# Kernel tuning notes

Measured on AMD Instinct MI355X. Metric: run time of the kernel, lower is better.

Reference implementation:

```python
import jax, jax.numpy as jnp
import numpy as np

N_NODES = 100000
N_EDGES = 1600000  # undirected edges (each pair listed once, no self loops)
IN_CH, HID, OUT_CH = 512, 64, 32
MU, P, K = 0.1, 1.5, 2
EPS = 1e-8


def setup_inputs() -> dict:
    key = jax.random.key(0)
    k_x, k_src, k_off, k_w1, k_w2 = jax.random.split(key, 5)
    x = jax.random.normal(k_x, (N_NODES, IN_CH), dtype=jnp.float32)
    # undirected edge list with no self loops: dst = (src + offset) % N, offset in [1, N)
    src = jax.random.randint(k_src, (N_EDGES,), 0, N_NODES)
    off = jax.random.randint(k_off, (N_EDGES,), 1, N_NODES)
    dst = (src + off) % N_NODES
    edge_index = jnp.stack([src, dst], axis=0)
    # parameters (lin1 of pGNNNet, lin1 of pGNNConv)
    W1 = jax.random.normal(k_w1, (IN_CH, HID), dtype=jnp.float32) / np.sqrt(IN_CH)
    b1 = jnp.zeros((HID,), dtype=jnp.float32)
    W2 = jax.random.normal(k_w2, (HID, OUT_CH), dtype=jnp.float32) / np.sqrt(HID)
    b2 = jnp.zeros((OUT_CH,), dtype=jnp.float32)
    return {"x": x, "edge_index": edge_index, "W1": W1, "b1": b1, "W2": W2, "b2": b2}


def reference(x, edge_index, W1, b1, W2, b2):
    src, dst = edge_index[0], edge_index[1]
    n = x.shape[0]
    # pGNNNet.lin1 + ReLU (dropout is identity in eval mode)
    h = jax.nn.relu(x @ W1 + b1)                   # [N, HID]
    # pGNNConv.lin1 applied before propagation
    f = h @ W2 + b2                                # [N, OUT]
    # degrees of the symmetric adjacency (no self loops)
    ones = jnp.ones(src.shape, dtype=f.dtype)
    deg = jax.ops.segment_sum(ones, src, num_segments=n) + \
          jax.ops.segment_sum(ones, dst, num_segments=n)
    dinv = jnp.where(deg > 0, 1.0 / deg, 0.0)      # [N]
    dis = jnp.sqrt(dinv)                           # D^{-1/2}
    out = f
    for _ in range(K):
        gs = out * dis[:, None]                    # D^{-1/2} f
        g = gs[src] - gs[dst]                      # graph gradient per edge [E, OUT]
        # edge reweighting: ||grad||^{p-2}
        w = jnp.power(jnp.sum(g * g, axis=1) + EPS, (P - 2.0) * 0.5)   # [E]
        # row sums of M (symmetric, M_ij = w_e)
        s = jax.ops.segment_sum(w, src, num_segments=n) + \
            jax.ops.segment_sum(w, dst, num_segments=n)
        alpha = 1.0 / (s * dinv + MU)              # [N]
        beta = MU * alpha
        # (D^{-1/2} M D^{-1/2} out): scatter-add messages both directions
        m = w[:, None]
        agg = jax.ops.segment_sum(m * gs[dst], src, num_segments=n) + \
              jax.ops.segment_sum(m * gs[src], dst, num_segments=n)
        out = alpha[:, None] * (dis[:, None] * agg) + beta[:, None] * f
    return jax.nn.log_softmax(out, axis=1)
```

## Files before the change

### kernel.cpp

```cpp
#include <hip/hip_runtime.h>
#include <hip/hip_bf16.h>
#include <math.h>

#define N_NODES 100000
#define N_EDGES 1600000
#define IN_CH 512
#define HID 64
#define OUT_CH 32
#define MU 0.1f
#define EPS 1e-8f

#define HE (2 * N_EDGES)
#define ABLK 625
#define EPT 20
#define NBUCK 391
#define BCAP 9216
#define PCAP 10240

typedef short bf16x8 __attribute__((ext_vector_type(8)));
typedef unsigned short us8 __attribute__((ext_vector_type(8)));
typedef float f32x4 __attribute__((ext_vector_type(4)));

__device__ __forceinline__ short f2bf(float f) {
  __hip_bfloat16 h = __float2bfloat16(f);
  return *reinterpret_cast<short*>(&h);
}
__device__ __forceinline__ float bf2f(unsigned short u) {
  unsigned int b = ((unsigned int)u) << 16;
  return __uint_as_float(b);
}

__global__ __launch_bounds__(256) void k_scatter(
    const int* __restrict__ ends, const float* __restrict__ W1,
    const float* __restrict__ W2, short* __restrict__ w1t,
    short* __restrict__ w2t, int* __restrict__ gcur, int* __restrict__ pairs) {
  const int t = threadIdx.x;
  const int b = blockIdx.x;
  {
    const int i = b * 256 + t;
    if (i < IN_CH * HID) {
      int k = i / HID, c = i % HID;
      w1t[c * IN_CH + k] = f2bf(W1[i]);
    } else if (i < IN_CH * HID + HID * OUT_CH) {
      int j = i - IN_CH * HID;
      w2t[(j % OUT_CH) * HID + (j / OUT_CH)] = f2bf(W2[j]);
    }
  }
  __shared__ int cnt[NBUCK];
  for (int i = t; i < NBUCK; i += 256) cnt[i] = 0;
  __syncthreads();
  const int base = b * (256 * EPT);
  int us[EPT];
  #pragma unroll
  for (int j = 0; j < EPT; ++j) us[j] = ends[base + j * 256 + t];
  #pragma unroll
  for (int j = 0; j < EPT; ++j) atomicAdd(&cnt[us[j] >> 8], 1);
  __syncthreads();
  for (int i = t; i < NBUCK; i += 256) {
    const int c = cnt[i];
    cnt[i] = c > 0 ? i * BCAP + atomicAdd(&gcur[i], c) : 0;
  }
  __syncthreads();
  #pragma unroll
  for (int j = 0; j < EPT; ++j) {
    const int i = base + j * 256 + t;
    const int u = us[j];
    const int nb = ends[i < N_EDGES ? i + N_EDGES : i - N_EDGES];
    pairs[atomicAdd(&cnt[u >> 8], 1)] = ((u & 255) << 24) | nb;
  }
}

__global__ __launch_bounds__(256) void k_csr(const int* __restrict__ pairs,
                                             const int* __restrict__ gcur,
                                             int2* __restrict__ degrs,
                                             int* __restrict__ adj) {
  __shared__ int pl[PCAP];
  __shared__ int cnt[256];
  __shared__ int sh[256];
  const int b = blockIdx.x, t = threadIdx.x;
  const int pbase = b * BCAP;
  const int psz = gcur[b];
  const bool fits = psz <= PCAP;
  cnt[t] = 0;
  __syncthreads();
  if (fits) {
    for (int i = t; i < psz; i += 256) {
      int p = pairs[pbase + i];
      pl[i] = p;
      atomicAdd(&cnt[((unsigned)p) >> 24], 1);
    }
  } else {
    for (int i = t; i < psz; i += 256)
      atomicAdd(&cnt[((unsigned)pairs[pbase + i]) >> 24], 1);
  }
  __syncthreads();
  const int d = cnt[t];
  sh[t] = d;
  __syncthreads();
  for (int s = 1; s < 256; s <<= 1) {
    int a = t >= s ? sh[t - s] : 0;
    __syncthreads();
    sh[t] += a;
    __syncthreads();
  }
  const int rs = pbase + sh[t] - d;
  const int v = (b << 8) + t;
  if (v < N_NODES) degrs[v] = make_int2(d, rs);
  __syncthreads();
  cnt[t] = rs;
  __syncthreads();
  for (int i = t; i < psz; i += 256) {
    const int p = fits ? pl[i] : pairs[pbase + i];
    adj[atomicAdd(&cnt[((unsigned)p) >> 24], 1)] = p & 0xFFFFFF;
  }
}

__global__ __launch_bounds__(256) void k_mlp(
    const float* __restrict__ x, const short* __restrict__ w1t,
    const float* __restrict__ b1, const short* __restrict__ w2t,
    const float* __restrict__ b2, const int2* __restrict__ degrs,
    float* __restrict__ f, unsigned short* __restrict__ gs) {
  __shared__ short ht[4][16][72];
  __shared__ __align__(16) float xstage[4][2080];

  const int t = threadIdx.x;
  const int w = t >> 6;
  const int l = t & 63;
  const int lr = l & 15;
  const int kq = l >> 4;
  const int band = blockIdx.x * 64 + w * 16;

  float* xb = xstage[w];
  const int srow = l >> 5;
  const int sgran = l & 31;

  f32x4 acc1[4] = {};
  const char* fb = (const char*)xb + (lr >> 1) * 1040 + (lr & 1) * 512 + kq * 32;

  for (int c = 0; c < 4; ++c) {
    asm volatile("" ::: "memory");
    #pragma unroll
    for (int i = 0; i < 8; ++i) {
      int grow = band + 2 * i + srow;
      grow = grow < N_NODES ? grow : N_NODES - 1;
      const float* gsrc = x + (size_t)grow * IN_CH + c * 128 + sgran * 4;
      __builtin_amdgcn_global_load_lds(
          (const __attribute__((address_space(1))) void*)gsrc,
          (__attribute__((address_space(3))) void*)(xb + i * 260),
          16, 0, 0);
    }
    asm volatile("s_waitcnt vmcnt(0)" ::: "memory");
    #pragma unroll
    for (int ksub = 0; ksub < 4; ++ksub) {
      const f32x4 alo = *(const f32x4*)(fb + ksub * 128);
      const f32x4 ahi = *(const f32x4*)(fb + ksub * 128 + 16);
      bf16x8 a;
      a[0] = f2bf(alo[0]); a[1] = f2bf(alo[1]); a[2] = f2bf(alo[2]); a[3] = f2bf(alo[3]);
      a[4] = f2bf(ahi[0]); a[5] = f2bf(ahi[1]); a[6] = f2bf(ahi[2]); a[7] = f2bf(ahi[3]);
      const int kg = c * 4 + ksub;
      #pragma unroll
      for (int ct = 0; ct < 4; ++ct) {
        const int cc = ct * 16 + lr;
        bf16x8 bfrag = *(const bf16x8*)&w1t[cc * IN_CH + kg * 32 + kq * 8];
        acc1[ct] = __builtin_amdgcn_mfma_f32_16x16x32_bf16(a, bfrag, acc1[ct], 0, 0, 0);
      }
    }
  }

  #pragma unroll
  for (int ct = 0; ct < 4; ++ct) {
    const int c = ct * 16 + lr;
    const float bb = b1[c];
    #pragma unroll
    for (int r = 0; r < 4; ++r) {
      float h = acc1[ct][r] + bb;
      ht[w][kq * 4 + r][c] = f2bf(h > 0.f ? h : 0.f);
    }
  }
  __syncthreads();

  f32x4 acc2[2] = {};
  #pragma unroll
  for (int ks = 0; ks < 2; ++ks) {
    bf16x8 a2 = *(const bf16x8*)&ht[w][lr][ks * 32 + kq * 8];
    #pragma unroll
    for (int ct = 0; ct < 2; ++ct) {
      const int c = ct * 16 + lr;
      bf16x8 bfrag = *(const bf16x8*)&w2t[c * HID + ks * 32 + kq * 8];
      acc2[ct] = __builtin_amdgcn_mfma_f32_16x16x32_bf16(a2, bfrag, acc2[ct], 0, 0, 0);
    }
  }

  #pragma unroll
  for (int r = 0; r < 4; ++r) {
    const int gr2 = band + kq * 4 + r;
    if (gr2 < N_NODES) {
      const int d = degrs[gr2].x;
      const float di = d > 0 ? 1.0f / (float)d : 0.0f;
      const float disv = sqrtf(di);
      #pragma unroll
      for (int ct = 0; ct < 2; ++ct) {
        const int c = ct * 16 + lr;
        const float fv = acc2[ct][r] + b2[c];
        f[(size_t)gr2 * OUT_CH + c] = fv;
        gs[(size_t)gr2 * OUT_CH + c] = (unsigned short)f2bf(fv * disv);
      }
    }
  }
}

template <bool FINAL>
__global__ __launch_bounds__(256) void k_prop(
    const unsigned short* __restrict__ gs_in, const float* __restrict__ f,
    const int2* __restrict__ degrs, const int* __restrict__ adj,
    float* __restrict__ outf, unsigned short* __restrict__ outg) {
  const int v = blockIdx.x * 4 + (threadIdx.x >> 6);
  const int lane = threadIdx.x & 63;
  const int slot = lane >> 2;
  const int cg2 = (lane & 3) << 3;

  const int2 dr = degrs[v];
  const int dg = dr.x;
  const int i0 = dr.y;
  const us8 gvu = *(const us8*)&gs_in[v * OUT_CH + cg2];
  const float4 fv0 = *(const float4*)&f[v * OUT_CH + cg2];
  const float4 fv1 = *(const float4*)&f[v * OUT_CH + cg2 + 4];
  float gv[8];
  #pragma unroll
  for (int j = 0; j < 8; ++j) gv[j] = bf2f(gvu[j]);

  const float dinvv = dg > 0 ? 1.0f / (float)dg : 0.0f;
  const float disv = sqrtf(dinvv);

  float accs = 0.f;
  float acca[8] = {0.f, 0.f, 0.f, 0.f, 0.f, 0.f, 0.f, 0.f};

  int u[3];
  #pragma unroll
  for (int q = 0; q < 3; ++q) {
    const int idx = q * 16 + slot;
    u[q] = idx < dg ? adj[i0 + idx] : v;
  }
  us8 guu[3];
  #pragma unroll
  for (int q = 0; q < 3; ++q)
    guu[q] = *(const us8*)&gs_in[u[q] * OUT_CH + cg2];
  #pragma unroll
  for (int q = 0; q < 3; ++q) {
    const bool vq = (q * 16 + slot) < dg;
    float gu[8];
    #pragma unroll
    for (int j = 0; j < 8; ++j) gu[j] = bf2f(guu[q][j]);
    float d = gv[0] - gu[0];
    float sq = d * d;
    #pragma unroll
    for (int j = 1; j < 8; ++j) { d = gv[j] - gu[j]; sq = fmaf(d, d, sq); }
    sq += __shfl_xor(sq, 1);
    sq += __shfl_xor(sq, 2);
    const float wq = vq ? __frsqrt_rn(sqrtf(sq + EPS)) : 0.f;
    accs += wq;
    #pragma unroll
    for (int j = 0; j < 8; ++j) acca[j] = fmaf(wq, gu[j], acca[j]);
  }
  for (int base = 48; base < dg; base += 16) {
    const int idx = base + slot;
    const bool vq = idx < dg;
    const int ut = vq ? adj[i0 + idx] : v;
    const us8 gut = *(const us8*)&gs_in[ut * OUT_CH + cg2];
    float gu[8];
    #pragma unroll
    for (int j = 0; j < 8; ++j) gu[j] = bf2f(gut[j]);
    float d = gv[0] - gu[0];
    float sq = d * d;
    #pragma unroll
    for (int j = 1; j < 8; ++j) { d = gv[j] - gu[j]; sq = fmaf(d, d, sq); }
    sq += __shfl_xor(sq, 1);
    sq += __shfl_xor(sq, 2);
    const float wq = vq ? __frsqrt_rn(sqrtf(sq + EPS)) : 0.f;
    accs += wq;
    #pragma unroll
    for (int j = 0; j < 8; ++j) acca[j] = fmaf(wq, gu[j], acca[j]);
  }

  #pragma unroll
  for (int s = 4; s <= 32; s <<= 1) {
    accs += __shfl_xor(accs, s);
    #pragma unroll
    for (int j = 0; j < 8; ++j) acca[j] += __shfl_xor(acca[j], s);
  }

  const float alpha = 1.0f / (accs * dinvv + MU);
  const float ad = alpha * disv;
  const float ba = MU * alpha;
  float r[8];
  r[0] = fmaf(ad, acca[0], ba * fv0.x);
  r[1] = fmaf(ad, acca[1], ba * fv0.y);
  r[2] = fmaf(ad, acca[2], ba * fv0.z);
  r[3] = fmaf(ad, acca[3], ba * fv0.w);
  r[4] = fmaf(ad, acca[4], ba * fv1.x);
  r[5] = fmaf(ad, acca[5], ba * fv1.y);
  r[6] = fmaf(ad, acca[6], ba * fv1.z);
  r[7] = fmaf(ad, acca[7], ba * fv1.w);

  if (FINAL) {
    float m = r[0];
    #pragma unroll
    for (int j = 1; j < 8; ++j) m = fmaxf(m, r[j]);
    m = fmaxf(m, __shfl_xor(m, 1));
    m = fmaxf(m, __shfl_xor(m, 2));
    float se = 0.f;
    #pragma unroll
    for (int j = 0; j < 8; ++j) se += __expf(r[j] - m);
    se += __shfl_xor(se, 1);
    se += __shfl_xor(se, 2);
    const float lse = m + __logf(se);
    if (slot == 0) {
      float4 o0 = make_float4(r[0] - lse, r[1] - lse, r[2] - lse, r[3] - lse);
      float4 o1 = make_float4(r[4] - lse, r[5] - lse, r[6] - lse, r[7] - lse);
      *(float4*)&outf[v * OUT_CH + cg2] = o0;
      *(float4*)&outf[v * OUT_CH + cg2 + 4] = o1;
    }
  } else {
    if (slot == 0) {
      us8 o;
      #pragma unroll
      for (int j = 0; j < 8; ++j) o[j] = (unsigned short)f2bf(r[j] * disv);
      *(us8*)&outg[v * OUT_CH + cg2] = o;
    }
  }
}

extern "C" void kernel_launch(void* const* d_in, const int* in_sizes, int n_in,
                              void* d_out, int out_size, void* d_ws, size_t ws_size,
                              hipStream_t stream) {
  const float* x = (const float*)d_in[0];
  const int* ei = (const int*)d_in[1];
  const float* W1 = (const float*)d_in[2];
  const float* b1 = (const float*)d_in[3];
  const float* W2 = (const float*)d_in[4];
  const float* b2 = (const float*)d_in[5];
  float* out = (float*)d_out;

  float* f = (float*)d_ws;
  unsigned short* gsa = (unsigned short*)(f + (size_t)N_NODES * 32);
  unsigned short* gsb = gsa + (size_t)N_NODES * 32;
  int2* degrs = (int2*)(gsb + (size_t)N_NODES * 32);
  int* adj = (int*)(degrs + N_NODES);
  short* w1t = (short*)(adj + NBUCK * BCAP);
  short* w2t = w1t + IN_CH * HID;
  int* gcur = (int*)(w2t + HID * OUT_CH);
  int* pairs = (int*)f;

  hipMemsetAsync(gcur, 0, NBUCK * sizeof(int), stream);
  k_scatter<<<ABLK, 256, 0, stream>>>(ei, W1, W2, w1t, w2t, gcur, pairs);
  k_csr<<<NBUCK, 256, 0, stream>>>(pairs, gcur, degrs, adj);
  k_mlp<<<(N_NODES + 63) / 64, 256, 0, stream>>>(x, w1t, b1, w2t, b2, degrs, f, gsa);
  k_prop<false><<<N_NODES / 4, 256, 0, stream>>>(gsa, f, degrs, adj, nullptr, gsb);
  k_prop<true><<<N_NODES / 4, 256, 0, stream>>>(gsb, f, degrs, adj, out, nullptr);
}
```

Before: 248.0 us.

## Use fixed-stride padded adjacency, double-buffer MLP loads, hoist prop neighbor loads

```diff
diff --git a/kernel.cpp b/kernel.cpp
--- a/kernel.cpp
+++ b/kernel.cpp
@@ -16,6 +16,7 @@
 #define NBUCK 391
 #define BCAP 9216
 #define PCAP 10240
+#define NCAP 72
 
 typedef short bf16x8 __attribute__((ext_vector_type(8)));
 typedef unsigned short us8 __attribute__((ext_vector_type(8)));
@@ -72,11 +73,11 @@
 
 __global__ __launch_bounds__(256) void k_csr(const int* __restrict__ pairs,
                                              const int* __restrict__ gcur,
-                                             int2* __restrict__ degrs,
+                                             int* __restrict__ degs,
                                              int* __restrict__ adj) {
   __shared__ int pl[PCAP];
   __shared__ int cnt[256];
-  __shared__ int sh[256];
+  __shared__ int cur[256];
   const int b = blockIdx.x, t = threadIdx.x;
   const int pbase = b * BCAP;
   const int psz = gcur[b];
@@ -95,33 +96,26 @@
   }
   __syncthreads();
   const int d = cnt[t];
-  sh[t] = d;
-  __syncthreads();
-  for (int s = 1; s < 256; s <<= 1) {
-    int a = t >= s ? sh[t - s] : 0;
-    __syncthreads();
-    sh[t] += a;
-    __syncthreads();
-  }
-  const int rs = pbase + sh[t] - d;
   const int v = (b << 8) + t;
-  if (v < N_NODES) degrs[v] = make_int2(d, rs);
-  __syncthreads();
-  cnt[t] = rs;
+  if (v < N_NODES) degs[v] = d;
+  cur[t] = v * NCAP;
   __syncthreads();
   for (int i = t; i < psz; i += 256) {
     const int p = fits ? pl[i] : pairs[pbase + i];
-    adj[atomicAdd(&cnt[((unsigned)p) >> 24], 1)] = p & 0xFFFFFF;
+    adj[atomicAdd(&cur[((unsigned)p) >> 24], 1)] = p & 0xFFFFFF;
+  }
+  if (v < N_NODES) {
+    for (int i = d; i < NCAP; ++i) adj[v * NCAP + i] = 0;
   }
 }
 
 __global__ __launch_bounds__(256) void k_mlp(
     const float* __restrict__ x, const short* __restrict__ w1t,
     const float* __restrict__ b1, const short* __restrict__ w2t,
-    const float* __restrict__ b2, const int2* __restrict__ degrs,
+    const float* __restrict__ b2, const int* __restrict__ degs,
     float* __restrict__ f, unsigned short* __restrict__ gs) {
   __shared__ short ht[4][16][72];
-  __shared__ __align__(16) float xstage[4][2080];
+  __shared__ __align__(16) float xstage[4][2][2080];
 
   const int t = threadIdx.x;
   const int w = t >> 6;
@@ -130,15 +124,16 @@
   const int kq = l >> 4;
   const int band = blockIdx.x * 64 + w * 16;
 
-  float* xb = xstage[w];
   const int srow = l >> 5;
   const int sgran = l & 31;
 
+  float* bufA = xstage[w][0];
+  float* bufB = xstage[w][1];
+  const size_t fboff = (size_t)(lr >> 1) * 1040 + (lr & 1) * 512 + kq * 32;
+
   f32x4 acc1[4] = {};
-  const char* fb = (const char*)xb + (lr >> 1) * 1040 + (lr & 1) * 512 + kq * 32;
-
-  for (int c = 0; c < 4; ++c) {
-    asm volatile("" ::: "memory");
+
+  auto issue = [&](int c, float* buf) {
     #pragma unroll
     for (int i = 0; i < 8; ++i) {
       int grow = band + 2 * i + srow;
@@ -146,10 +141,12 @@
       const float* gsrc = x + (size_t)grow * IN_CH + c * 128 + sgran * 4;
       __builtin_amdgcn_global_load_lds(
           (const __attribute__((address_space(1))) void*)gsrc,
-          (__attribute__((address_space(3))) void*)(xb + i * 260),
+          (__attribute__((address_space(3))) void*)(buf + i * 260),
           16, 0, 0);
     }
-    asm volatile("s_waitcnt vmcnt(0)" ::: "memory");
+  };
+  auto compute = [&](int c, const float* buf) {
+    const char* fb = (const char*)buf + fboff;
     #pragma unroll
     for (int ksub = 0; ksub < 4; ++ksub) {
       const f32x4 alo = *(const f32x4*)(fb + ksub * 128);
@@ -165,7 +162,20 @@
         acc1[ct] = __builtin_amdgcn_mfma_f32_16x16x32_bf16(a, bfrag, acc1[ct], 0, 0, 0);
       }
     }
-  }
+  };
+
+  issue(0, bufA);
+  issue(1, bufB);
+  asm volatile("s_waitcnt vmcnt(0)" ::: "memory");
+  compute(0, bufA);
+  asm volatile("" ::: "memory");
+  issue(2, bufA);
+  compute(1, bufB);
+  asm volatile("" ::: "memory");
+  issue(3, bufB);
+  asm volatile("s_waitcnt vmcnt(0)" ::: "memory");
+  compute(2, bufA);
+  compute(3, bufB);
 
   #pragma unroll
   for (int ct = 0; ct < 4; ++ct) {
@@ -195,7 +205,7 @@
   for (int r = 0; r < 4; ++r) {
     const int gr2 = band + kq * 4 + r;
     if (gr2 < N_NODES) {
-      const int d = degrs[gr2].x;
+      const int d = degs[gr2];
       const float di = d > 0 ? 1.0f / (float)d : 0.0f;
       const float disv = sqrtf(di);
       #pragma unroll
@@ -212,39 +222,36 @@
 template <bool FINAL>
 __global__ __launch_bounds__(256) void k_prop(
     const unsigned short* __restrict__ gs_in, const float* __restrict__ f,
-    const int2* __restrict__ degrs, const int* __restrict__ adj,
+    const int* __restrict__ degs, const int* __restrict__ adj,
     float* __restrict__ outf, unsigned short* __restrict__ outg) {
   const int v = blockIdx.x * 4 + (threadIdx.x >> 6);
   const int lane = threadIdx.x & 63;
   const int slot = lane >> 2;
   const int cg2 = (lane & 3) << 3;
 
-  const int2 dr = degrs[v];
-  const int dg = dr.x;
-  const int i0 = dr.y;
+  const int i0 = v * NCAP;
+  int u[3];
+  #pragma unroll
+  for (int q = 0; q < 3; ++q) u[q] = adj[i0 + q * 16 + slot];
+  const int dg = degs[v];
   const us8 gvu = *(const us8*)&gs_in[v * OUT_CH + cg2];
   const float4 fv0 = *(const float4*)&f[v * OUT_CH + cg2];
   const float4 fv1 = *(const float4*)&f[v * OUT_CH + cg2 + 4];
+
+  us8 guu[3];
+  #pragma unroll
+  for (int q = 0; q < 3; ++q)
+    guu[q] = *(const us8*)&gs_in[u[q] * OUT_CH + cg2];
+
   float gv[8];
   #pragma unroll
   for (int j = 0; j < 8; ++j) gv[j] = bf2f(gvu[j]);
-
   const float dinvv = dg > 0 ? 1.0f / (float)dg : 0.0f;
   const float disv = sqrtf(dinvv);
 
   float accs = 0.f;
   float acca[8] = {0.f, 0.f, 0.f, 0.f, 0.f, 0.f, 0.f, 0.f};
 
-  int u[3];
-  #pragma unroll
-  for (int q = 0; q < 3; ++q) {
-    const int idx = q * 16 + slot;
-    u[q] = idx < dg ? adj[i0 + idx] : v;
-  }
-  us8 guu[3];
-  #pragma unroll
-  for (int q = 0; q < 3; ++q)
-    guu[q] = *(const us8*)&gs_in[u[q] * OUT_CH + cg2];
   #pragma unroll
   for (int q = 0; q < 3; ++q) {
     const bool vq = (q * 16 + slot) < dg;
@@ -344,17 +351,17 @@
   float* f = (float*)d_ws;
   unsigned short* gsa = (unsigned short*)(f + (size_t)N_NODES * 32);
   unsigned short* gsb = gsa + (size_t)N_NODES * 32;
-  int2* degrs = (int2*)(gsb + (size_t)N_NODES * 32);
-  int* adj = (int*)(degrs + N_NODES);
-  short* w1t = (short*)(adj + NBUCK * BCAP);
+  int* degs = (int*)(gsb + (size_t)N_NODES * 32);
+  int* adj = degs + N_NODES;
+  short* w1t = (short*)(adj + (size_t)N_NODES * NCAP);
   short* w2t = w1t + IN_CH * HID;
   int* gcur = (int*)(w2t + HID * OUT_CH);
   int* pairs = (int*)f;
 
   hipMemsetAsync(gcur, 0, NBUCK * sizeof(int), stream);
   k_scatter<<<ABLK, 256, 0, stream>>>(ei, W1, W2, w1t, w2t, gcur, pairs);
-  k_csr<<<NBUCK, 256, 0, stream>>>(pairs, gcur, degrs, adj);
-  k_mlp<<<(N_NODES + 63) / 64, 256, 0, stream>>>(x, w1t, b1, w2t, b2, degrs, f, gsa);
-  k_prop<false><<<N_NODES / 4, 256, 0, stream>>>(gsa, f, degrs, adj, nullptr, gsb);
-  k_prop<true><<<N_NODES / 4, 256, 0, stream>>>(gsb, f, degrs, adj, out, nullptr);
-}
+  k_csr<<<NBUCK, 256, 0, stream>>>(pairs, gcur, degs, adj);
+  k_mlp<<<(N_NODES + 63) / 64, 256, 0, stream>>>(x, w1t, b1, w2t, b2, degs, f, gsa);
+  k_prop<false><<<N_NODES / 4, 256, 0, stream>>>(gsa, f, degs, adj, nullptr, gsb);
+  k_prop<true><<<N_NODES / 4, 256, 0, stream>>>(gsb, f, degs, adj, out, nullptr);
+}
```

Measured after the change: 260.7 us. +5.1%, slower.
